# Kernel tuning notes

Measured on AMD Instinct MI355X. Metric: run time of the kernel, lower is better.

The kernel has to match this reference:

```python
import jax, jax.numpy as jnp
import numpy as np

B, H, S, DK, DV = 4, 16, 2048, 64, 64
D_K = 64  # config.d_k used for scaling

def setup_inputs() -> dict:
    key = jax.random.key(0)
    kq, kk, kv, km = jax.random.split(key, 4)
    Q = jax.random.normal(kq, (B, H, S, DK), dtype=jnp.float32)
    K = jax.random.normal(kk, (B, H, S, DK), dtype=jnp.float32)
    V = jax.random.normal(kv, (B, H, S, DV), dtype=jnp.float32)
    attn_mask = jax.random.randint(km, (B, 1, S, S), 0, 2).astype(jnp.bool_)
    return {"Q": Q, "K": K, "V": V, "attn_mask": attn_mask}

def reference(Q, K, V, attn_mask):
    # scores: [B, H, S, S]
    scale = 1.0 / jnp.sqrt(jnp.asarray(D_K, dtype=Q.dtype))
    scores = jnp.einsum("bhqd,bhkd->bhqk", Q, K) * scale
    scores = jnp.where(attn_mask, jnp.asarray(-1e9, dtype=scores.dtype), scores)
    attn = jax.nn.softmax(scores, axis=-1)
    context = jnp.einsum("bhqk,bhkv->bhqv", attn, V)
    return context
```

## Files before the change

kernel.cpp:

```cpp
#include <hip/hip_runtime.h>
#include <hip/hip_bf16.h>
#include <math.h>

typedef __attribute__((ext_vector_type(4)))  float f32x4;
typedef __attribute__((ext_vector_type(16))) float f32x16;
typedef __attribute__((ext_vector_type(8)))  short short8_t;
typedef __attribute__((ext_vector_type(4)))  short short4_t;

constexpr int Bn = 4, Hn = 16, Sn = 2048, Dn = 64;
constexpr int MW  = Sn / 64;
constexpr int NKT = Sn / 64;

__device__ __forceinline__ unsigned short f2bf(float f) {
    union { float f; unsigned u; } x; x.f = f;
    unsigned r = x.u + 0x7fffu + ((x.u >> 16) & 1u);
    return (unsigned short)(r >> 16);
}
__device__ __forceinline__ int sw8(int row) { return (row ^ (row >> 3)) & 7; }
__device__ __forceinline__ float exp2fast(float x) {
#if __has_builtin(__builtin_amdgcn_exp2f)
    return __builtin_amdgcn_exp2f(x);
#else
    float r; asm("v_exp_f32 %0, %1" : "=v"(r) : "v"(x)); return r;
#endif
}
__device__ __forceinline__ float max3f(float a, float b, float c) {
    return fmaxf(fmaxf(a, b), c);
}
__device__ __forceinline__ f32x16 zero16() {
    f32x16 z;
#pragma unroll
    for (int i = 0; i < 16; ++i) z[i] = 0.f;
    return z;
}
__device__ __forceinline__ unsigned cvtpk(float lo, float hi_) {
    __hip_bfloat162 h2 = __float22bfloat162_rn(make_float2(lo, hi_));
    union { __hip_bfloat162 h; unsigned u; } u; u.h = h2;
    return u.u;
}
__device__ __forceinline__ void pswap(unsigned &x, unsigned &y) {
    asm("v_permlane32_swap_b32 %0, %1" : "+v"(x), "+v"(y));
}

__global__ __launch_bounds__(256) void pack_mask(const void* __restrict__ Mp,
                                                 unsigned long long* __restrict__ PM) {
    unsigned accv = 0;
    {
        const unsigned* mw = (const unsigned*)Mp;
#pragma unroll
        for (int i = 0; i < 8; ++i) accv |= (mw[i] & 0xFFFFFF00u);
    }
    const bool i32 = (accv == 0u);
    const int lane = threadIdx.x & 63;
    const int wv = (int)((blockIdx.x * 256 + threadIdx.x) >> 6);
    const int w0 = wv * (Bn * Sn * MW / 4096);
    const int* mi32 = (const int*)Mp;
    const unsigned char* mu8 = (const unsigned char*)Mp;
    for (int j = 0; j < 64; j += 4) {
        int m0, m1, m2, m3;
        if (i32) {
            m0 = mi32[(size_t)(w0 + j) * 64 + lane];
            m1 = mi32[(size_t)(w0 + j + 1) * 64 + lane];
            m2 = mi32[(size_t)(w0 + j + 2) * 64 + lane];
            m3 = mi32[(size_t)(w0 + j + 3) * 64 + lane];
        } else {
            m0 = mu8[(size_t)(w0 + j) * 64 + lane];
            m1 = mu8[(size_t)(w0 + j + 1) * 64 + lane];
            m2 = mu8[(size_t)(w0 + j + 2) * 64 + lane];
            m3 = mu8[(size_t)(w0 + j + 3) * 64 + lane];
        }
        unsigned long long b0 = __ballot(m0 != 0);
        unsigned long long b1 = __ballot(m1 != 0);
        unsigned long long b2 = __ballot(m2 != 0);
        unsigned long long b3 = __ballot(m3 != 0);
        if (lane == 0) {
            PM[w0 + j] = b0; PM[w0 + j + 1] = b1;
            PM[w0 + j + 2] = b2; PM[w0 + j + 3] = b3;
        }
    }
}

__global__ __launch_bounds__(256) void convKV(const float* __restrict__ K,
                                              const float* __restrict__ V,
                                              unsigned short* __restrict__ Kb,
                                              unsigned short* __restrict__ Vt) {
    __shared__ unsigned short tile[64 * 72];
    const int bh = blockIdx.x, kt = blockIdx.y, t = threadIdx.x;

    {
        const float* ksrc = K + ((size_t)bh * Sn + kt * 64) * 64;
        unsigned short* kdst = Kb + ((size_t)bh * Sn + kt * 64) * 64;
#pragma unroll
        for (int j = 0; j < 2; ++j) {
            const int idx = j * 256 + t;
            f32x4 a = *(const f32x4*)(ksrc + idx * 8);
            f32x4 b = *(const f32x4*)(ksrc + idx * 8 + 4);
            short8_t h;
            h[0]=(short)f2bf(a[0]); h[1]=(short)f2bf(a[1]); h[2]=(short)f2bf(a[2]); h[3]=(short)f2bf(a[3]);
            h[4]=(short)f2bf(b[0]); h[5]=(short)f2bf(b[1]); h[6]=(short)f2bf(b[2]); h[7]=(short)f2bf(b[3]);
            *(short8_t*)(kdst + idx * 8) = h;
        }
    }

    {
        const int k = t >> 2, vq = (t & 3) * 16;
        const float* src = V + ((size_t)bh * Sn + kt * 64 + k) * 64 + vq;
#pragma unroll
        for (int j = 0; j < 4; ++j) {
            f32x4 f = *(const f32x4*)(src + j * 4);
            short4_t h;
            h[0]=(short)f2bf(f[0]); h[1]=(short)f2bf(f[1]); h[2]=(short)f2bf(f[2]); h[3]=(short)f2bf(f[3]);
            *(short4_t*)&tile[k * 72 + vq + j * 4] = h;
        }
        __syncthreads();
#pragma unroll
        for (int j = 0; j < 2; ++j) {
            const int v = (t >> 3) + 32 * j;
            const int oct = t & 7;
            short8_t h;
#pragma unroll
            for (int i2 = 0; i2 < 8; ++i2) h[i2] = (short)tile[(oct * 8 + i2) * 72 + v];
            *(short8_t*)(Vt + ((size_t)bh * 64 + v) * Sn + kt * 64 + oct * 8) = h;
        }
    }
}

__global__ __launch_bounds__(256, 3) void sdpa_v3(
    const float* __restrict__ Qp, const unsigned short* __restrict__ Kb,
    const unsigned short* __restrict__ Vt, const unsigned long long* __restrict__ PM,
    float* __restrict__ Op)
{
    __shared__ __align__(16) char smem[32768];
    unsigned short* smK = (unsigned short*)smem;
    unsigned short* smV = (unsigned short*)(smem + 16384);
    unsigned short* smQ = (unsigned short*)smem;

    const int t = threadIdx.x;
    const int w = t >> 6;
    const int l = t & 63;
    const int ql = l & 31;
    const int hi = l >> 5;

    const int gid = blockIdx.x;
    const int lin = (gid & 7) * 128 + (gid >> 3);
    const int bh = lin >> 4;
    const int qb = lin & 15;
    const int b = bh >> 4;
    const int q0 = qb * 128;

    const unsigned short* KbB = Kb + (size_t)bh * Sn * 64;
    const unsigned short* VtB = Vt + (size_t)bh * 64 * Sn;

    {
        const float qscale = 0.125f * 1.44269504088896340736f;
        const float* Qbase = Qp + ((size_t)bh * Sn + q0) * Dn;
#pragma unroll
        for (int j = 0; j < 8; ++j) {
            const int flat = j * 256 + t;
            const int row = flat >> 4, c4 = (flat & 15) * 4;
            f32x4 f = *(const f32x4*)(Qbase + (size_t)flat * 4);
            short4_t h;
            h[0]=(short)f2bf(f[0]*qscale); h[1]=(short)f2bf(f[1]*qscale);
            h[2]=(short)f2bf(f[2]*qscale); h[3]=(short)f2bf(f[3]*qscale);
            *(short4_t*)&smQ[row * 72 + c4] = h;
        }
    }
    __syncthreads();
    short8_t qf[4];
    {
        const int rowl = w * 32 + ql;
#pragma unroll
        for (int tt = 0; tt < 4; ++tt)
            qf[tt] = *(const short8_t*)&smQ[rowl * 72 + tt * 16 + hi * 8];
    }
    __syncthreads();

    auto stage = [&](int kt, int buf) {
        const int row = t >> 3, oct = t & 7;
        const int row2 = row + 32;
        {
            const unsigned short* g = KbB + ((size_t)(kt * 64 + row)) * 64 + (oct ^ sw8(row)) * 8;
            __builtin_amdgcn_global_load_lds((const __attribute__((address_space(1))) unsigned int*)g,
                (__attribute__((address_space(3))) unsigned int*)(smK + buf * 4096 + t * 8), 16, 0, 0);
            const unsigned short* g2 = KbB + ((size_t)(kt * 64 + row2)) * 64 + (oct ^ sw8(row2)) * 8;
            __builtin_amdgcn_global_load_lds((const __attribute__((address_space(1))) unsigned int*)g2,
                (__attribute__((address_space(3))) unsigned int*)(smK + buf * 4096 + 2048 + t * 8), 16, 0, 0);
        }
        {
            const unsigned short* g = VtB + (size_t)row * Sn + kt * 64 + (oct ^ sw8(row)) * 8;
            __builtin_amdgcn_global_load_lds((const __attribute__((address_space(1))) unsigned int*)g,
                (__attribute__((address_space(3))) unsigned int*)(smV + buf * 4096 + t * 8), 16, 0, 0);
            const unsigned short* g2 = VtB + (size_t)row2 * Sn + kt * 64 + (oct ^ sw8(row2)) * 8;
            __builtin_amdgcn_global_load_lds((const __attribute__((address_space(1))) unsigned int*)g2,
                (__attribute__((address_space(3))) unsigned int*)(smV + buf * 4096 + 2048 + t * 8), 16, 0, 0);
        }
    };
    auto ldf = [&](const unsigned short* base, int row, int olog) -> short8_t {
        return *(const short8_t*)(base + row * 64 + (olog ^ sw8(row)) * 8);
    };

    f32x16 o0 = zero16(), o1 = zero16();
    float m_run = -INFINITY, l_run = 0.f;
    const int qrow = q0 + w * 32 + ql;
    const unsigned long long* pmrow = PM + ((size_t)b * Sn + qrow) * MW;

    stage(0, 0);
    __syncthreads();

    for (int kt = 0; kt < NKT; ++kt) {
        const int cur = kt & 1;
        if (kt + 1 < NKT) stage(kt + 1, cur ^ 1);
        const unsigned long long bits = pmrow[kt];
        const unsigned short* bK = smK + cur * 4096;
        const unsigned short* bV = smV + cur * 4096;

        f32x16 s0 = zero16(), s1 = zero16();
        __builtin_amdgcn_s_setprio(1);
#pragma unroll
        for (int tt = 0; tt < 4; ++tt) {
            short8_t a0 = ldf(bK, ql,      2 * tt + hi);
            short8_t a1 = ldf(bK, 32 + ql, 2 * tt + hi);
            s0 = __builtin_amdgcn_mfma_f32_32x32x16_bf16(a0, qf[tt], s0, 0, 0, 0);
            s1 = __builtin_amdgcn_mfma_f32_32x32x16_bf16(a1, qf[tt], s1, 0, 0, 0);
        }
        __builtin_amdgcn_s_setprio(0);

        const unsigned long long bb = bits >> (hi * 4);
        const unsigned blo = (unsigned)bb, bhi = (unsigned)(bb >> 32);
#pragma unroll
        for (int r = 0; r < 16; ++r) {
            const int bp = 8 * (r >> 2) + (r & 3);
            s0[r] = ((blo >> bp) & 1u) ? -1e9f : s0[r];
            s1[r] = ((bhi >> bp) & 1u) ? -1e9f : s1[r];
        }

        float mx0 = fmaxf(s0[0], s0[1]);
        float mx1 = fmaxf(s1[0], s1[1]);
#pragma unroll
        for (int r = 2; r < 16; r += 2) {
            mx0 = max3f(mx0, s0[r], s0[r + 1]);
            mx1 = max3f(mx1, s1[r], s1[r + 1]);
        }
        float mx = fmaxf(mx0, mx1);
        mx = fmaxf(mx, __shfl_xor(mx, 32));

        if (!__all(mx - m_run <= 8.0f)) {
            const float mn = fmaxf(m_run, mx);
            const float corr = exp2fast(m_run - mn);
            m_run = mn;
            l_run *= corr;
#pragma unroll
            for (int r = 0; r < 16; ++r) {
                const int qloc = (r & 3) + 8 * (r >> 2) + 4 * hi;
                const float cr = __shfl(corr, qloc);
                o0[r] *= cr; o1[r] *= cr;
            }
        }
#pragma unroll
        for (int r = 0; r < 16; ++r) {
            s0[r] = exp2fast(s0[r] - m_run);
            s1[r] = exp2fast(s1[r] - m_run);
        }

        {
            float p0 = 0.f, p1 = 0.f, p2 = 0.f, p3 = 0.f;
#pragma unroll
            for (int r = 0; r < 16; r += 4) {
                p0 += s0[r];     p1 += s0[r + 1]; p2 += s0[r + 2]; p3 += s0[r + 3];
                p0 += s1[r];     p1 += s1[r + 1]; p2 += s1[r + 2]; p3 += s1[r + 3];
            }
            float rs = (p0 + p1) + (p2 + p3);
            rs += __shfl_xor(rs, 32);
            l_run += rs;
        }

        __builtin_amdgcn_s_setprio(1);
#pragma unroll
        for (int ks = 0; ks < 4; ++ks) {
            const f32x16& sv = (ks < 2) ? s0 : s1;
            const int off = (ks & 1) * 8;
            unsigned x0 = cvtpk(sv[off],     sv[off + 1]);
            unsigned x1 = cvtpk(sv[off + 2], sv[off + 3]);
            unsigned y0 = cvtpk(sv[off + 4], sv[off + 5]);
            unsigned y1 = cvtpk(sv[off + 6], sv[off + 7]);
            pswap(x0, y0);
            pswap(x1, y1);
            union { unsigned u[4]; short8_t v; } pa;
            pa.u[0] = x0; pa.u[1] = x1; pa.u[2] = y0; pa.u[3] = y1;
            short8_t vf0 = ldf(bV, ql,      2 * ks + hi);
            short8_t vf1 = ldf(bV, 32 + ql, 2 * ks + hi);
            o0 = __builtin_amdgcn_mfma_f32_32x32x16_bf16(pa.v, vf0, o0, 0, 0, 0);
            o1 = __builtin_amdgcn_mfma_f32_32x32x16_bf16(pa.v, vf1, o1, 0, 0, 0);
        }
        __builtin_amdgcn_s_setprio(0);
        __syncthreads();
    }

    const float inv = 1.0f / l_run;
#pragma unroll
    for (int r = 0; r < 16; ++r) {
        const int qloc = (r & 3) + 8 * (r >> 2) + 4 * hi;
        const float iv = __shfl(inv, qloc);
        float* orow = Op + ((size_t)bh * Sn + q0 + w * 32 + qloc) * 64;
        orow[ql] = o0[r] * iv;
        orow[32 + ql] = o1[r] * iv;
    }
}

__global__ __launch_bounds__(512, 4) void sdpa_v2(
    const float* __restrict__ Qp, const float* __restrict__ Kp,
    const float* __restrict__ Vp, const void* __restrict__ Mp,
    const unsigned long long* __restrict__ PM, float* __restrict__ Op)
{
    __shared__ unsigned short lds_k[64 * 64];
    __shared__ unsigned short lds_vt[64 * 64];
    __shared__ unsigned short lds_p[8][16 * 64];

    const int t = threadIdx.x;
    const int wave = t >> 6;
    const int lane = t & 63;
    const int g = lane >> 4;
    const int c = lane & 15;

    const int gid = blockIdx.x;
    const int lin = (gid & 7) * 128 + (gid >> 3);
    const int bh = lin >> 4;
    const int qb = lin & 15;
    const int b = bh >> 4;
    const int q0 = qb * 128;

    bool m_i32 = true;
    if (!PM) {
        unsigned accv = 0;
        const unsigned* mw = (const unsigned*)Mp;
#pragma unroll
        for (int i = 0; i < 32; ++i) accv |= (mw[i] & 0xFFFFFF00u);
        m_i32 = (accv == 0u);
    }
    const int* mi32 = (const int*)Mp;
    const unsigned char* mu8 = (const unsigned char*)Mp;

    short8_t qf[2];
    {
        const float qscale = 0.125f * 1.44269504088896340736f;
        const float* qsrc = Qp + ((size_t)bh * Sn + q0 + wave * 16 + c) * Dn + g * 8;
#pragma unroll
        for (int h2 = 0; h2 < 2; ++h2) {
            f32x4 f0 = *(const f32x4*)(qsrc + h2 * 32);
            f32x4 f1 = *(const f32x4*)(qsrc + h2 * 32 + 4);
            short8_t v;
            v[0]=(short)f2bf(f0[0]*qscale); v[1]=(short)f2bf(f0[1]*qscale);
            v[2]=(short)f2bf(f0[2]*qscale); v[3]=(short)f2bf(f0[3]*qscale);
            v[4]=(short)f2bf(f1[0]*qscale); v[5]=(short)f2bf(f1[1]*qscale);
            v[6]=(short)f2bf(f1[2]*qscale); v[7]=(short)f2bf(f1[3]*qscale);
            qf[h2] = v;
        }
    }

    f32x4 o[4];
#pragma unroll
    for (int i = 0; i < 4; ++i) o[i] = (f32x4){0.f, 0.f, 0.f, 0.f};
    float m_run[4] = {-INFINITY, -INFINITY, -INFINITY, -INFINITY};
    float l_run[4] = {0.f, 0.f, 0.f, 0.f};

    const float* kbase = Kp + (size_t)bh * Sn * Dn;
    const float* vbase = Vp + (size_t)bh * Sn * Dn;
    const size_t mrow0 = (size_t)b * Sn + q0 + wave * 16 + g * 4;

    for (int kt = 0; kt < NKT; ++kt) {
        const int k0 = kt * 64;
        {
            const int key = t >> 3;
            const int d0 = (t & 7) * 8;
            const float* src = kbase + (size_t)(k0 + key) * Dn + d0;
            f32x4 f0 = *(const f32x4*)src;
            f32x4 f1 = *(const f32x4*)(src + 4);
            short8_t hv;
            hv[0]=(short)f2bf(f0[0]); hv[1]=(short)f2bf(f0[1]);
            hv[2]=(short)f2bf(f0[2]); hv[3]=(short)f2bf(f0[3]);
            hv[4]=(short)f2bf(f1[0]); hv[5]=(short)f2bf(f1[1]);
            hv[6]=(short)f2bf(f1[2]); hv[7]=(short)f2bf(f1[3]);
            *(short8_t*)&lds_k[key * 64 + (d0 ^ (sw8(key) << 3))] = hv;
        }
        {
            const int vv = t & 63;
            const int kq = (t >> 6) * 8;
            short8_t hv;
#pragma unroll
            for (int j = 0; j < 8; ++j)
                hv[j] = (short)f2bf(vbase[(size_t)(k0 + kq + j) * Dn + vv]);
            *(short8_t*)&lds_vt[vv * 64 + (kq ^ (sw8(vv) << 3))] = hv;
        }
        __syncthreads();

        f32x4 s[4];
#pragma unroll
        for (int e = 0; e < 4; ++e) s[e] = (f32x4){0.f, 0.f, 0.f, 0.f};
        __builtin_amdgcn_s_setprio(1);
#pragma unroll
        for (int e = 0; e < 4; ++e) {
            const int ke = e * 16 + c;
            const int swk = sw8(ke) << 3;
            short8_t kf0 = *(const short8_t*)&lds_k[ke * 64 + ((g * 8) ^ swk)];
            short8_t kf1 = *(const short8_t*)&lds_k[ke * 64 + ((32 + g * 8) ^ swk)];
            s[e] = __builtin_amdgcn_mfma_f32_16x16x32_bf16(qf[0], kf0, s[e], 0, 0, 0);
            s[e] = __builtin_amdgcn_mfma_f32_16x16x32_bf16(qf[1], kf1, s[e], 0, 0, 0);
        }
        __builtin_amdgcn_s_setprio(0);

        unsigned long long bits[4];
        if (PM) {
#pragma unroll
            for (int r = 0; r < 4; ++r) bits[r] = PM[(mrow0 + r) * MW + kt];
        } else {
#pragma unroll
            for (int r = 0; r < 4; ++r) {
                const size_t mi = (mrow0 + r) * Sn + k0 + c;
                unsigned long long bbv = 0;
#pragma unroll
                for (int e = 0; e < 4; ++e) {
                    int mm = m_i32 ? mi32[mi + 16 * e] : (int)mu8[mi + 16 * e];
                    bbv |= (unsigned long long)(mm != 0) << (c + 16 * e);
                }
                bits[r] = bbv;
            }
        }

        float p[4][4], mx[4];
#pragma unroll
        for (int r = 0; r < 4; ++r) {
            const unsigned lo = (unsigned)bits[r];
            const unsigned hh = (unsigned)(bits[r] >> 32);
            const unsigned t0 = lo >> c;
            const unsigned t1 = hh >> c;
            float v0 = (t0 & 1u)       ? -1e9f : s[0][r];
            float v1 = (t0 & 0x10000u) ? -1e9f : s[1][r];
            float v2 = (t1 & 1u)       ? -1e9f : s[2][r];
            float v3 = (t1 & 0x10000u) ? -1e9f : s[3][r];
            p[0][r] = v0; p[1][r] = v1; p[2][r] = v2; p[3][r] = v3;
            mx[r] = fmaxf(fmaxf(v0, v1), fmaxf(v2, v3));
        }
#pragma unroll
        for (int sh = 1; sh < 16; sh <<= 1) {
#pragma unroll
            for (int r = 0; r < 4; ++r) mx[r] = fmaxf(mx[r], __shfl_xor(mx[r], sh));
        }
        float need = mx[0] - m_run[0];
        need = fmaxf(need, mx[1] - m_run[1]);
        need = fmaxf(need, mx[2] - m_run[2]);
        need = fmaxf(need, mx[3] - m_run[3]);
        if (!__all(need <= 8.0f)) {
#pragma unroll
            for (int r = 0; r < 4; ++r) {
                const float mn = fmaxf(m_run[r], mx[r]);
                const float corr = exp2fast(m_run[r] - mn);
                m_run[r] = mn;
                l_run[r] *= corr;
#pragma unroll
                for (int cg = 0; cg < 4; ++cg) o[cg][r] *= corr;
            }
        }
        float rsv[4];
#pragma unroll
        for (int r = 0; r < 4; ++r) {
            p[0][r] = exp2fast(p[0][r] - m_run[r]);
            p[1][r] = exp2fast(p[1][r] - m_run[r]);
            p[2][r] = exp2fast(p[2][r] - m_run[r]);
            p[3][r] = exp2fast(p[3][r] - m_run[r]);
            rsv[r] = (p[0][r] + p[1][r]) + (p[2][r] + p[3][r]);
        }
#pragma unroll
        for (int sh = 1; sh < 16; sh <<= 1) {
#pragma unroll
            for (int r = 0; r < 4; ++r) rsv[r] += __shfl_xor(rsv[r], sh);
        }
#pragma unroll
        for (int r = 0; r < 4; ++r) l_run[r] += rsv[r];

        unsigned short* pw = lds_p[wave];
#pragma unroll
        for (int r = 0; r < 4; ++r) {
            const int row = g * 4 + r;
            const int swp = sw8(row) << 3;
            pw[row * 64 + ((c)      ^ swp)] = f2bf(p[0][r]);
            pw[row * 64 + ((c + 16) ^ swp)] = f2bf(p[1][r]);
            pw[row * 64 + ((c + 32) ^ swp)] = f2bf(p[2][r]);
            pw[row * 64 + ((c + 48) ^ swp)] = f2bf(p[3][r]);
        }
        const int swc = sw8(c) << 3;
        const short8_t pf0 = *(const short8_t*)&pw[c * 64 + ((g * 8) ^ swc)];
        const short8_t pf1 = *(const short8_t*)&pw[c * 64 + ((32 + g * 8) ^ swc)];
        __builtin_amdgcn_s_setprio(1);
#pragma unroll
        for (int cg = 0; cg < 4; ++cg) {
            const int vv = cg * 16 + c;
            const int swv = sw8(vv) << 3;
            const short8_t vf0 = *(const short8_t*)&lds_vt[vv * 64 + ((g * 8) ^ swv)];
            const short8_t vf1 = *(const short8_t*)&lds_vt[vv * 64 + ((32 + g * 8) ^ swv)];
            o[cg] = __builtin_amdgcn_mfma_f32_16x16x32_bf16(pf0, vf0, o[cg], 0, 0, 0);
            o[cg] = __builtin_amdgcn_mfma_f32_16x16x32_bf16(pf1, vf1, o[cg], 0, 0, 0);
        }
        __builtin_amdgcn_s_setprio(0);
        __syncthreads();
    }

#pragma unroll
    for (int r = 0; r < 4; ++r) {
        const float inv = 1.0f / l_run[r];
        float* orow = Op + ((size_t)bh * Sn + q0 + wave * 16 + g * 4 + r) * Dn + c;
#pragma unroll
        for (int cg = 0; cg < 4; ++cg) orow[cg * 16] = o[cg][r] * inv;
    }
}

extern "C" void kernel_launch(void* const* d_in, const int* in_sizes, int n_in,
                              void* d_out, int out_size, void* d_ws, size_t ws_size,
                              hipStream_t stream) {
    (void)in_sizes; (void)n_in; (void)out_size;
    const float* Q = (const float*)d_in[0];
    const float* K = (const float*)d_in[1];
    const float* V = (const float*)d_in[2];
    const void*  M = d_in[3];
    float* O = (float*)d_out;

    const size_t pmB = (size_t)Bn * Sn * MW * 8;
    const size_t kvB = (size_t)Bn * Hn * Sn * Dn * 2;

    if (ws_size >= pmB + 2 * kvB) {
        unsigned long long* PM = (unsigned long long*)d_ws;
        unsigned short* Kb = (unsigned short*)((char*)d_ws + pmB);
        unsigned short* Vt = (unsigned short*)((char*)d_ws + pmB + kvB);
        pack_mask<<<1024, 256, 0, stream>>>(M, PM);
        convKV<<<dim3(Bn * Hn, NKT), 256, 0, stream>>>(K, V, Kb, Vt);
        sdpa_v3<<<dim3(1024), dim3(256), 0, stream>>>(Q, Kb, Vt, PM, O);
    } else {
        unsigned long long* PM = nullptr;
        if (ws_size >= pmB) {
            PM = (unsigned long long*)d_ws;
            pack_mask<<<1024, 256, 0, stream>>>(M, PM);
        }
        sdpa_v2<<<dim3(1024), dim3(512), 0, stream>>>(Q, K, V, M, PM, O);
    }
}
```

Baseline: 145.1 us.

## Split 64-key tile into two 32-key halves to cut registers, raise occupancy

Each 64-key tile is now processed as two 32-key sub-tiles, each running its own QK MFMA, mask, online-softmax update and PV MFMA. Only one 16-float score accumulator is live instead of two, and the launch bound is raised from 3 to 4 waves per SIMD so more blocks can be resident. The cost is twice as many max/sum shuffles and rescale checks per tile, and shorter MFMA chains that give less instruction-level parallelism.

After: 145.1 us. No clear change (+0.0%).

```diff
diff --git a/kernel.cpp b/kernel.cpp
--- a/kernel.cpp
+++ b/kernel.cpp
@@ -125,7 +125,7 @@
     }
 }
 
-__global__ __launch_bounds__(256, 3) void sdpa_v3(
+__global__ __launch_bounds__(256, 4) void sdpa_v3(
     const float* __restrict__ Qp, const unsigned short* __restrict__ Kb,
     const unsigned short* __restrict__ Vt, const unsigned long long* __restrict__ PM,
     float* __restrict__ Op)
@@ -214,85 +214,75 @@
         const unsigned short* bK = smK + cur * 4096;
         const unsigned short* bV = smV + cur * 4096;
 
-        f32x16 s0 = zero16(), s1 = zero16();
-        __builtin_amdgcn_s_setprio(1);
-#pragma unroll
-        for (int tt = 0; tt < 4; ++tt) {
-            short8_t a0 = ldf(bK, ql,      2 * tt + hi);
-            short8_t a1 = ldf(bK, 32 + ql, 2 * tt + hi);
-            s0 = __builtin_amdgcn_mfma_f32_32x32x16_bf16(a0, qf[tt], s0, 0, 0, 0);
-            s1 = __builtin_amdgcn_mfma_f32_32x32x16_bf16(a1, qf[tt], s1, 0, 0, 0);
-        }
-        __builtin_amdgcn_s_setprio(0);
-
-        const unsigned long long bb = bits >> (hi * 4);
-        const unsigned blo = (unsigned)bb, bhi = (unsigned)(bb >> 32);
-#pragma unroll
-        for (int r = 0; r < 16; ++r) {
-            const int bp = 8 * (r >> 2) + (r & 3);
-            s0[r] = ((blo >> bp) & 1u) ? -1e9f : s0[r];
-            s1[r] = ((bhi >> bp) & 1u) ? -1e9f : s1[r];
-        }
-
-        float mx0 = fmaxf(s0[0], s0[1]);
-        float mx1 = fmaxf(s1[0], s1[1]);
-#pragma unroll
-        for (int r = 2; r < 16; r += 2) {
-            mx0 = max3f(mx0, s0[r], s0[r + 1]);
-            mx1 = max3f(mx1, s1[r], s1[r + 1]);
-        }
-        float mx = fmaxf(mx0, mx1);
-        mx = fmaxf(mx, __shfl_xor(mx, 32));
-
-        if (!__all(mx - m_run <= 8.0f)) {
-            const float mn = fmaxf(m_run, mx);
-            const float corr = exp2fast(m_run - mn);
-            m_run = mn;
-            l_run *= corr;
+#pragma unroll
+        for (int h = 0; h < 2; ++h) {
+            f32x16 s = zero16();
+            __builtin_amdgcn_s_setprio(1);
+#pragma unroll
+            for (int tt = 0; tt < 4; ++tt) {
+                short8_t a0 = ldf(bK, 32 * h + ql, 2 * tt + hi);
+                s = __builtin_amdgcn_mfma_f32_32x32x16_bf16(a0, qf[tt], s, 0, 0, 0);
+            }
+            __builtin_amdgcn_s_setprio(0);
+
+            const unsigned w32 = (unsigned)(bits >> (32 * h)) >> (hi * 4);
 #pragma unroll
             for (int r = 0; r < 16; ++r) {
-                const int qloc = (r & 3) + 8 * (r >> 2) + 4 * hi;
-                const float cr = __shfl(corr, qloc);
-                o0[r] *= cr; o1[r] *= cr;
-            }
-        }
-#pragma unroll
-        for (int r = 0; r < 16; ++r) {
-            s0[r] = exp2fast(s0[r] - m_run);
-            s1[r] = exp2fast(s1[r] - m_run);
-        }
-
-        {
-            float p0 = 0.f, p1 = 0.f, p2 = 0.f, p3 = 0.f;
-#pragma unroll
-            for (int r = 0; r < 16; r += 4) {
-                p0 += s0[r];     p1 += s0[r + 1]; p2 += s0[r + 2]; p3 += s0[r + 3];
-                p0 += s1[r];     p1 += s1[r + 1]; p2 += s1[r + 2]; p3 += s1[r + 3];
-            }
-            float rs = (p0 + p1) + (p2 + p3);
-            rs += __shfl_xor(rs, 32);
-            l_run += rs;
-        }
-
-        __builtin_amdgcn_s_setprio(1);
-#pragma unroll
-        for (int ks = 0; ks < 4; ++ks) {
-            const f32x16& sv = (ks < 2) ? s0 : s1;
-            const int off = (ks & 1) * 8;
-            unsigned x0 = cvtpk(sv[off],     sv[off + 1]);
-            unsigned x1 = cvtpk(sv[off + 2], sv[off + 3]);
-            unsigned y0 = cvtpk(sv[off + 4], sv[off + 5]);
-            unsigned y1 = cvtpk(sv[off + 6], sv[off + 7]);
-            pswap(x0, y0);
-            pswap(x1, y1);
-            union { unsigned u[4]; short8_t v; } pa;
-            pa.u[0] = x0; pa.u[1] = x1; pa.u[2] = y0; pa.u[3] = y1;
-            short8_t vf0 = ldf(bV, ql,      2 * ks + hi);
-            short8_t vf1 = ldf(bV, 32 + ql, 2 * ks + hi);
-            o0 = __builtin_amdgcn_mfma_f32_32x32x16_bf16(pa.v, vf0, o0, 0, 0, 0);
-            o1 = __builtin_amdgcn_mfma_f32_32x32x16_bf16(pa.v, vf1, o1, 0, 0, 0);
-        }
-        __builtin_amdgcn_s_setprio(0);
+                const int bp = 8 * (r >> 2) + (r & 3);
+                s[r] = ((w32 >> bp) & 1u) ? -1e9f : s[r];
+            }
+
+            float mx = fmaxf(s[0], s[1]);
+#pragma unroll
+            for (int r = 2; r < 16; r += 2) mx = max3f(mx, s[r], s[r + 1]);
+            mx = fmaxf(mx, __shfl_xor(mx, 32));
+
+            if (!__all(mx - m_run <= 8.0f)) {
+                const float mn = fmaxf(m_run, mx);
+                const float corr = exp2fast(m_run - mn);
+                m_run = mn;
+                l_run *= corr;
+#pragma unroll
+                for (int r = 0; r < 16; ++r) {
+                    const int qloc = (r & 3) + 8 * (r >> 2) + 4 * hi;
+                    const float cr = __shfl(corr, qloc);
+                    o0[r] *= cr; o1[r] *= cr;
+                }
+            }
+#pragma unroll
+            for (int r = 0; r < 16; ++r) s[r] = exp2fast(s[r] - m_run);
+
+            {
+                float p0 = 0.f, p1 = 0.f, p2 = 0.f, p3 = 0.f;
+#pragma unroll
+                for (int r = 0; r < 16; r += 4) {
+                    p0 += s[r]; p1 += s[r + 1]; p2 += s[r + 2]; p3 += s[r + 3];
+                }
+                float rs = (p0 + p1) + (p2 + p3);
+                rs += __shfl_xor(rs, 32);
+                l_run += rs;
+            }
+
+            __builtin_amdgcn_s_setprio(1);
+#pragma unroll
+            for (int ksl = 0; ksl < 2; ++ksl) {
+                const int off = ksl * 8;
+                unsigned x0 = cvtpk(s[off],     s[off + 1]);
+                unsigned x1 = cvtpk(s[off + 2], s[off + 3]);
+                unsigned y0 = cvtpk(s[off + 4], s[off + 5]);
+                unsigned y1 = cvtpk(s[off + 6], s[off + 7]);
+                pswap(x0, y0);
+                pswap(x1, y1);
+                union { unsigned u[4]; short8_t v; } pa;
+                pa.u[0] = x0; pa.u[1] = x1; pa.u[2] = y0; pa.u[3] = y1;
+                const int ksg = 2 * h + ksl;
+                short8_t vf0 = ldf(bV, ql,      2 * ksg + hi);
+                short8_t vf1 = ldf(bV, 32 + ql, 2 * ksg + hi);
+                o0 = __builtin_amdgcn_mfma_f32_32x32x16_bf16(pa.v, vf0, o0, 0, 0, 0);
+                o1 = __builtin_amdgcn_mfma_f32_32x32x16_bf16(pa.v, vf1, o1, 0, 0, 0);
+            }
+            __builtin_amdgcn_s_setprio(0);
+        }
         __syncthreads();
     }
 
```
